# Optimization experiments

Measured on AMD Instinct MI355X. Metric: run time of the kernel, lower is better.

The kernel has to match this reference:

```python
import jax, jax.numpy as jnp
import numpy as np
import math

B, T, D, H = 4, 2048, 1024, 16
HD = D // H  # head_dim = 64

def setup_inputs() -> dict:
    key = jax.random.key(0)
    k1, k2, k3, k4, k5 = jax.random.split(key, 5)
    s = 1.0 / math.sqrt(D)
    return {
        "x": jax.random.normal(k1, (B, T, D), dtype=jnp.float32),
        "W_qkv": jax.random.normal(k2, (D, 3 * D), dtype=jnp.float32) * s,
        "b_qkv": jax.random.normal(k3, (3 * D,), dtype=jnp.float32) * 0.01,
        "W_fc": jax.random.normal(k4, (D, D), dtype=jnp.float32) * s,
        "b_fc": jax.random.normal(k5, (D,), dtype=jnp.float32) * 0.01,
    }

def reference(x, W_qkv, b_qkv, W_fc, b_fc):
    Bx, Tx, C = x.shape
    qkv = x @ W_qkv + b_qkv                                   # [B,T,3D]
    qkv = qkv.reshape(Bx, Tx, 3, H, HD)
    q, k, v = qkv[:, :, 0], qkv[:, :, 1], qkv[:, :, 2]        # [B,T,H,hd]
    scale = 1.0 / math.sqrt(HD)
    scores = jnp.einsum('bqhd,bkhd->bhqk', q, k) * scale      # [B,H,T,T]
    causal = jnp.tril(jnp.ones((Tx, Tx), dtype=bool))
    scores = jnp.where(causal, scores, -jnp.inf)
    weights = jax.nn.softmax(scores, axis=-1)
    out = jnp.einsum('bhqk,bkhd->bqhd', weights, v).reshape(Bx, Tx, C)
    return out @ W_fc + b_fc
```

## Files before the change

kernel.cpp:

```cpp
#include <hip/hip_runtime.h>
#include <hip/hip_bf16.h>

typedef __hip_bfloat16 bf16;
typedef short bf16x8 __attribute__((ext_vector_type(8)));
typedef float f32x4 __attribute__((ext_vector_type(4)));


static __device__ __forceinline__ void glds16(const bf16* g, bf16* l) {
  __builtin_amdgcn_global_load_lds(
      (const __attribute__((address_space(1))) void*)g,
      (__attribute__((address_space(3))) void*)l, 16, 0, 0);
}

static __device__ __forceinline__ unsigned short f2b(float f) {
  return __builtin_bit_cast(unsigned short, __float2bfloat16(f));
}
static __device__ __forceinline__ float b2f(unsigned int u16bits) {
  return __builtin_bit_cast(float, u16bits << 16);
}
static __device__ __forceinline__ float ex2(float x) {
  return __builtin_amdgcn_exp2f(x);
}

__global__ void k_convert(const float* __restrict__ in, unsigned short* __restrict__ out, int n4) {
  int i = blockIdx.x * 256 + threadIdx.x;
  if (i >= n4) return;
  float4 v = reinterpret_cast<const float4*>(in)[i];
  ushort4 o;
  o.x = f2b(v.x); o.y = f2b(v.y); o.z = f2b(v.z); o.w = f2b(v.w);
  reinterpret_cast<ushort4*>(out)[i] = o;
}

__global__ void k_transpose(const float* __restrict__ in, bf16* __restrict__ out, int R, int C) {
  __shared__ float t[32][33];
  int c0 = blockIdx.x * 32, r0 = blockIdx.y * 32;
  int tx = threadIdx.x, ty = threadIdx.y;
  #pragma unroll
  for (int j = 0; j < 32; j += 8)
    t[ty + j][tx] = in[(size_t)(r0 + ty + j) * C + c0 + tx];
  __syncthreads();
  #pragma unroll
  for (int j = 0; j < 32; j += 8)
    out[(size_t)(c0 + ty + j) * R + r0 + tx] = __float2bfloat16(t[tx][ty + j]);
}

template<int EPI>
__global__ __launch_bounds__(256, 2)
void k_gemm(const bf16* __restrict__ A, const bf16* __restrict__ Bt,
            const float* __restrict__ bias,
            bf16* __restrict__ Qh, bf16* __restrict__ Kh, bf16* __restrict__ Vt,
            float* __restrict__ Out)
{
  constexpr int K = 1024;
  __shared__ bf16 sA[128 * 64];
  __shared__ bf16 sB[128 * 64];
  const int tid = threadIdx.x;
  const int wv = tid >> 6, lane = tid & 63;
  const int wr = wv >> 1, wc = wv & 1;
  const int l4 = lane >> 4, l15 = lane & 15;

  const int nbx = gridDim.x;
  const int nwg = nbx * gridDim.y;
  const int flat = blockIdx.y * nbx + blockIdx.x;
  const int cpx = nwg >> 3;
  const int swz = (flat & 7) * cpx + (flat >> 3);
  const int bx = swz % nbx;
  const int by = swz / nbx;

  const int srow8 = lane >> 3;
  const int sgran = (lane & 7) ^ srow8;
  const bf16* gA0 = A  + (size_t)(by * 128 + wv * 8 + srow8) * K + sgran * 8;
  const bf16* gB0 = Bt + (size_t)(bx * 128 + wv * 8 + srow8) * K + sgran * 8;
  bf16* lA0 = sA + wv * 8 * 64;
  bf16* lB0 = sB + wv * 8 * 64;

  f32x4 acc[4][4];
  #pragma unroll
  for (int i = 0; i < 4; ++i)
    #pragma unroll
    for (int j = 0; j < 4; ++j) acc[i][j] = f32x4{0.f, 0.f, 0.f, 0.f};

  for (int kb = 0; kb < K; kb += 64) {
    #pragma unroll
    for (int c = 0; c < 4; ++c) {
      glds16(gA0 + kb + (size_t)(c * 32) * K, lA0 + c * 32 * 64);
      glds16(gB0 + kb + (size_t)(c * 32) * K, lB0 + c * 32 * 64);
    }
    __syncthreads();
    #pragma unroll
    for (int kk = 0; kk < 2; ++kk) {
      bf16x8 af[4], bfr[4];
      #pragma unroll
      for (int i = 0; i < 4; ++i) {
        const int R = wr * 64 + i * 16 + l15;
        af[i] = *reinterpret_cast<const bf16x8*>(
            sA + R * 64 + (((kk * 4 + l4) ^ (R & 7)) * 8));
      }
      #pragma unroll
      for (int j = 0; j < 4; ++j) {
        const int R = wc * 64 + j * 16 + l15;
        bfr[j] = *reinterpret_cast<const bf16x8*>(
            sB + R * 64 + (((kk * 4 + l4) ^ (R & 7)) * 8));
      }
      #pragma unroll
      for (int i = 0; i < 4; ++i)
        #pragma unroll
        for (int j = 0; j < 4; ++j)
          acc[i][j] = __builtin_amdgcn_mfma_f32_16x16x32_bf16(af[i], bfr[j], acc[i][j], 0, 0, 0);
    }
    __syncthreads();
  }

  if (EPI == 0) {
    #pragma unroll
    for (int j = 0; j < 4; ++j) {
      const int n = bx * 128 + wc * 64 + j * 16 + l15;
      const float bj = bias[n];
      const int s = n >> 10;
      const int hh = (n >> 6) & 15;
      const int d = n & 63;
      #pragma unroll
      for (int i = 0; i < 4; ++i) {
        #pragma unroll
        for (int r = 0; r < 4; ++r) {
          const int m = by * 128 + wr * 64 + i * 16 + l4 * 4 + r;
          const int bb = m >> 11, t = m & 2047;
          float of = acc[i][j][r] + bj;
          if (s == 0) of *= 0.18033688f;
          const bf16 o = __float2bfloat16(of);
          if (s == 0)      Qh[((size_t)((bb * 16 + hh) * 2048 + t)) * 64 + d] = o;
          else if (s == 1) Kh[((size_t)((bb * 16 + hh) * 2048 + t)) * 64 + d] = o;
          else             Vt[((size_t)((bb * 16 + hh) * 64 + d)) * 2048 + t] = o;
        }
      }
    }
  } else {
    #pragma unroll
    for (int j = 0; j < 4; ++j) {
      const int n = bx * 128 + wc * 64 + j * 16 + l15;
      const float bj = bias[n];
      #pragma unroll
      for (int i = 0; i < 4; ++i)
        #pragma unroll
        for (int r = 0; r < 4; ++r) {
          const int m = by * 128 + wr * 64 + i * 16 + l4 * 4 + r;
          Out[(size_t)m * 1024 + n] = acc[i][j][r] + bj;
        }
    }
  }
}

__global__ __launch_bounds__(256, 3)
void k_attn(const bf16* __restrict__ Qh, const bf16* __restrict__ Kh,
            const bf16* __restrict__ Vt, bf16* __restrict__ Ao)
{
  __shared__ unsigned int smem[4608];
  const int tid = threadIdx.x;
  const int wv = tid >> 6, lane = tid & 63;
  const int l4 = lane >> 4, l15 = lane & 15;

  const int bid = blockIdx.x;
  const int xcd = bid & 7;
  const int idx = bid >> 3;
  const int g   = idx & 31;
  const int grp = idx >> 5;
  const int bh  = grp * 8 + xcd;
  const int b = bh >> 4, h = bh & 15;

  const int role = (wv + bid) & 3;
  const int qi = (role < 2) ? g : (63 - g);
  const int parity = role & 1;
  const int qbase = qi * 32;

  const bf16* Qp = Qh + (size_t)bh * 2048 * 64;
  const bf16* Kp = Kh + (size_t)bh * 2048 * 64;
  const bf16* Vp = Vt + (size_t)bh * 64 * 2048;
  bf16* Pw = (bf16*)smem + wv * (32 * 40);

  bf16x8 qa[2][2];
  #pragma unroll
  for (int i = 0; i < 2; ++i)
    #pragma unroll
    for (int kh = 0; kh < 2; ++kh)
      qa[i][kh] = *reinterpret_cast<const bf16x8*>(
          Qp + (size_t)(qbase + i * 16 + l15) * 64 + kh * 32 + l4 * 8);

  f32x4 o[2][4];
  float mr[2], lr[2];
  #pragma unroll
  for (int i = 0; i < 2; ++i) {
    #pragma unroll
    for (int jd = 0; jd < 4; ++jd) o[i][jd] = f32x4{0.f, 0.f, 0.f, 0.f};
    mr[i] = -1e30f; lr[i] = 0.f;
  }

  const int ktmax = (qbase + 31) >> 5;

  const int kt0 = (parity <= ktmax) ? parity : ktmax;
  bf16x8 kbf[2][2];
  #pragma unroll
  for (int j = 0; j < 2; ++j)
    #pragma unroll
    for (int kh = 0; kh < 2; ++kh)
      kbf[j][kh] = *reinterpret_cast<const bf16x8*>(
          Kp + (size_t)(kt0 * 32 + j * 16 + l15) * 64 + kh * 32 + l4 * 8);

  for (int kt = parity; kt <= ktmax; kt += 2) {
    const bool full = (kt * 32 + 31) <= qbase;

    f32x4 s[2][2];
    #pragma unroll
    for (int i = 0; i < 2; ++i)
      #pragma unroll
      for (int j = 0; j < 2; ++j) s[i][j] = f32x4{0.f, 0.f, 0.f, 0.f};
    #pragma unroll
    for (int j = 0; j < 2; ++j)
      #pragma unroll
      for (int i = 0; i < 2; ++i) {
        s[i][j] = __builtin_amdgcn_mfma_f32_16x16x32_bf16(kbf[j][0], qa[i][0], s[i][j], 0, 0, 0);
        s[i][j] = __builtin_amdgcn_mfma_f32_16x16x32_bf16(kbf[j][1], qa[i][1], s[i][j], 0, 0, 0);
      }

    bf16x8 vbf[4];
    #pragma unroll
    for (int jd = 0; jd < 4; ++jd)
      vbf[jd] = *reinterpret_cast<const bf16x8*>(
          Vp + (size_t)(jd * 16 + l15) * 2048 + kt * 32 + l4 * 8);

    #pragma unroll
    for (int i = 0; i < 2; ++i) {
      const int q = qbase + i * 16 + l15;
      #pragma unroll
      for (int j = 0; j < 2; ++j)
        #pragma unroll
        for (int r = 0; r < 4; ++r) {
          float v = s[i][j][r];
          if (!full) {
            const int kk = kt * 32 + j * 16 + l4 * 4 + r;
            if (kk > q) v = -1e30f;
          }
          s[i][j][r] = v;
        }
    }

    #pragma unroll
    for (int i = 0; i < 2; ++i) {
      float mx = s[i][0][0];
      #pragma unroll
      for (int j = 0; j < 2; ++j)
        #pragma unroll
        for (int r = 0; r < 4; ++r)
          if (j + r > 0) mx = fmaxf(mx, s[i][j][r]);
      mx = fmaxf(mx, __shfl_xor(mx, 16));
      mx = fmaxf(mx, __shfl_xor(mx, 32));
      if (__any(mx > mr[i] + 8.f)) {
        const float mn = fmaxf(mr[i], mx);
        const float al = ex2(mr[i] - mn);
        mr[i] = mn;
        lr[i] *= al;
        float albc[4];
        #pragma unroll
        for (int r = 0; r < 4; ++r) albc[r] = __shfl(al, l4 * 4 + r);
        #pragma unroll
        for (int jd = 0; jd < 4; ++jd)
          #pragma unroll
          for (int r = 0; r < 4; ++r) o[i][jd][r] *= albc[r];
      }
      float ps = 0.f;
      #pragma unroll
      for (int j = 0; j < 2; ++j) {
        const float p0 = ex2(s[i][j][0] - mr[i]);
        const float p1 = ex2(s[i][j][1] - mr[i]);
        const float p2 = ex2(s[i][j][2] - mr[i]);
        const float p3 = ex2(s[i][j][3] - mr[i]);
        ps += (p0 + p1) + (p2 + p3);
        const unsigned int u0 = (unsigned int)f2b(p0) | ((unsigned int)f2b(p1) << 16);
        const unsigned int u1 = (unsigned int)f2b(p2) | ((unsigned int)f2b(p3) << 16);
        *reinterpret_cast<uint2*>(Pw + (i * 16 + l15) * 40 + j * 16 + l4 * 4) =
            make_uint2(u0, u1);
      }
      ps += __shfl_xor(ps, 16);
      ps += __shfl_xor(ps, 32);
      lr[i] += ps;
    }

    const int ktn = (kt + 2 <= ktmax) ? (kt + 2) : ktmax;
    #pragma unroll
    for (int j = 0; j < 2; ++j)
      #pragma unroll
      for (int kh = 0; kh < 2; ++kh)
        kbf[j][kh] = *reinterpret_cast<const bf16x8*>(
            Kp + (size_t)(ktn * 32 + j * 16 + l15) * 64 + kh * 32 + l4 * 8);

    bf16x8 pa[2];
    #pragma unroll
    for (int i = 0; i < 2; ++i)
      pa[i] = *reinterpret_cast<const bf16x8*>(Pw + (i * 16 + l15) * 40 + l4 * 8);
    #pragma unroll
    for (int jd = 0; jd < 4; ++jd)
      #pragma unroll
      for (int i = 0; i < 2; ++i)
        o[i][jd] = __builtin_amdgcn_mfma_f32_16x16x32_bf16(pa[i], vbf[jd], o[i][jd], 0, 0, 0);
  }

  float mrv[2][4], lrv[2][4];
  #pragma unroll
  for (int i = 0; i < 2; ++i)
    #pragma unroll
    for (int r = 0; r < 4; ++r) {
      mrv[i][r] = __shfl(mr[i], l4 * 4 + r);
      lrv[i][r] = __shfl(lr[i], l4 * 4 + r);
    }

  __syncthreads();
  unsigned int* reg0 = smem;
  unsigned int* reg1 = smem + 64 * 33;
  if (parity == 1) {
    unsigned int* p = ((role == 1) ? reg0 : reg1) + lane * 33;
    #pragma unroll
    for (int i = 0; i < 2; ++i)
      #pragma unroll
      for (int r = 0; r < 4; ++r) {
        p[i * 4 + r]     = __builtin_bit_cast(unsigned int, mrv[i][r]);
        p[8 + i * 4 + r] = __builtin_bit_cast(unsigned int, lrv[i][r]);
      }
    #pragma unroll
    for (int i = 0; i < 2; ++i)
      #pragma unroll
      for (int jd = 0; jd < 4; ++jd)
        #pragma unroll
        for (int rp = 0; rp < 2; ++rp) {
          unsigned int lo = f2b(o[i][jd][2 * rp]);
          unsigned int hi = f2b(o[i][jd][2 * rp + 1]);
          p[16 + (i * 4 + jd) * 2 + rp] = lo | (hi << 16);
        }
  }
  __syncthreads();
  if (parity == 0) {
    const unsigned int* p = ((role == 0) ? reg0 : reg1) + lane * 33;
    #pragma unroll
    for (int i = 0; i < 2; ++i)
      #pragma unroll
      for (int r = 0; r < 4; ++r) {
        const float m1 = __builtin_bit_cast(float, p[i * 4 + r]);
        const float l1 = __builtin_bit_cast(float, p[8 + i * 4 + r]);
        const float mm = fmaxf(mrv[i][r], m1);
        const float a0 = ex2(mrv[i][r] - mm);
        const float a1 = ex2(m1 - mm);
        const float inv = 1.f / (lrv[i][r] * a0 + l1 * a1);
        const int q = qbase + i * 16 + l4 * 4 + r;
        #pragma unroll
        for (int jd = 0; jd < 4; ++jd) {
          const unsigned int u = p[16 + (i * 4 + jd) * 2 + (r >> 1)];
          const float o1 = b2f((r & 1) ? (u >> 16) : (u & 0xffffu));
          const float val = (o[i][jd][r] * a0 + o1 * a1) * inv;
          Ao[(size_t)(b * 2048 + q) * 1024 + h * 64 + jd * 16 + l15] = __float2bfloat16(val);
        }
      }
  }
}

extern "C" void kernel_launch(void* const* d_in, const int* in_sizes, int n_in,
                              void* d_out, int out_size, void* d_ws, size_t ws_size,
                              hipStream_t stream)
{
  const float* x     = (const float*)d_in[0];
  const float* W_qkv = (const float*)d_in[1];
  const float* b_qkv = (const float*)d_in[2];
  const float* W_fc  = (const float*)d_in[3];
  const float* b_fc  = (const float*)d_in[4];
  float* out = (float*)d_out;

  char* ws = (char*)d_ws;
  bf16* x_bf = (bf16*)ws;  ws += (size_t)8192 * 1024 * 2;
  bf16* Wqt  = (bf16*)ws;  ws += (size_t)3072 * 1024 * 2;
  bf16* Wft  = (bf16*)ws;  ws += (size_t)1024 * 1024 * 2;
  bf16* Qh   = (bf16*)ws;  ws += (size_t)4 * 16 * 2048 * 64 * 2;
  bf16* Kh   = (bf16*)ws;  ws += (size_t)4 * 16 * 2048 * 64 * 2;
  bf16* Vt   = (bf16*)ws;  ws += (size_t)4 * 16 * 64 * 2048 * 2;
  bf16* Ao   = (bf16*)ws;  ws += (size_t)8192 * 1024 * 2;

  k_convert<<<8192, 256, 0, stream>>>(x, (unsigned short*)x_bf, 8192 * 1024 / 4);
  k_transpose<<<dim3(3072 / 32, 1024 / 32), dim3(32, 8), 0, stream>>>(W_qkv, Wqt, 1024, 3072);
  k_transpose<<<dim3(1024 / 32, 1024 / 32), dim3(32, 8), 0, stream>>>(W_fc, Wft, 1024, 1024);
  k_gemm<0><<<dim3(24, 64), 256, 0, stream>>>(x_bf, Wqt, b_qkv, Qh, Kh, Vt, nullptr);
  k_attn<<<2048, 256, 0, stream>>>(Qh, Kh, Vt, Ao);
  k_gemm<1><<<dim3(8, 64), 256, 0, stream>>>(Ao, Wft, b_fc, nullptr, nullptr, nullptr, out);
}
```

Measured before the change: 265.8 us.

## Replace QKV GEMM with 256x256-tile double-buffered pipelined kernel

The QKV projection moves to a new kernel with 256x256 output tiles, 8 waves per block and 128KB of dynamic LDS holding two K-stages. Global-to-LDS loads for the next stages are issued between MFMA phases, with explicit vmcnt waits, barriers and s_setprio, so memory traffic overlaps compute. The larger tile doubles reuse of each staged operand. The risks are one block per CU, higher register pressure from 32 accumulators per wave, and fragile hand-tuned wait counts. The output projection stays on the old kernel, now specialised as k_gemm_fc.

After: 268.7 us. Within noise of the previous version (+1.1%).

```diff
diff --git a/kernel.cpp b/kernel.cpp
--- a/kernel.cpp
+++ b/kernel.cpp
@@ -44,12 +44,135 @@
     out[(size_t)(c0 + ty + j) * R + r0 + tx] = __float2bfloat16(t[tx][ty + j]);
 }
 
-template<int EPI>
+__global__ __launch_bounds__(512, 1)
+void k_gemm2(const bf16* __restrict__ A, const bf16* __restrict__ Bt,
+             const float* __restrict__ bias,
+             bf16* __restrict__ Qh, bf16* __restrict__ Kh, bf16* __restrict__ Vt)
+{
+  constexpr int K = 1024, NT = 16;
+  extern __shared__ bf16 sm[];
+  #define BUFA(bb) (sm + (bb) * 2 * 16384)
+  #define BUFB(bb) (sm + (bb) * 2 * 16384 + 16384)
+
+  const int tid = threadIdx.x;
+  const int wv = tid >> 6, lane = tid & 63;
+  const int wr = wv >> 2, wc = wv & 3;
+  const int l4 = lane >> 4, l15 = lane & 15;
+
+  const int flat = blockIdx.x;
+  const int swz = (flat & 7) * 48 + (flat >> 3);
+  const int bx = swz % 12;
+  const int by = swz / 12;
+
+  const int srow = lane >> 3;
+  const int sgran = (lane & 7) ^ srow;
+  const bf16* gA = A  + (size_t)(by * 256 + wv * 8 + srow) * K + sgran * 8;
+  const bf16* gB = Bt + (size_t)(bx * 256 + wv * 8 + srow) * K + sgran * 8;
+
+  f32x4 acc[8][4];
+  #pragma unroll
+  for (int i = 0; i < 8; ++i)
+    #pragma unroll
+    for (int j = 0; j < 4; ++j) acc[i][j] = f32x4{0.f, 0.f, 0.f, 0.f};
+
+  #define STAGE_A(t, c, bb) glds16(gA + (size_t)((c) * 64) * K + (t) * 64, BUFA(bb) + ((c) * 64 + wv * 8) * 64)
+  #define STAGE_B(t, c, bb) glds16(gB + (size_t)((c) * 64) * K + (t) * 64, BUFB(bb) + ((c) * 64 + wv * 8) * 64)
+
+  #pragma unroll
+  for (int c = 0; c < 4; ++c) STAGE_A(0, c, 0);
+  #pragma unroll
+  for (int c = 0; c < 4; ++c) STAGE_B(0, c, 0);
+  #pragma unroll
+  for (int c = 0; c < 4; ++c) STAGE_B(1, c, 1);
+  STAGE_A(1, 0, 1);
+  STAGE_A(1, 2, 1);
+  asm volatile("s_waitcnt vmcnt(6)");
+  __builtin_amdgcn_sched_barrier(0);
+  __builtin_amdgcn_s_barrier();
+  __builtin_amdgcn_sched_barrier(0);
+
+  for (int h = 0; h < NT; ++h) {
+    const int b = h & 1;
+    bf16x8 bfr[4][2];
+    #pragma unroll
+    for (int p = 0; p < 4; ++p) {
+      if (p == 0) {
+        #pragma unroll
+        for (int j = 0; j < 4; ++j)
+          #pragma unroll
+          for (int kh = 0; kh < 2; ++kh) {
+            const int R = wc * 64 + j * 16 + l15;
+            bfr[j][kh] = *reinterpret_cast<const bf16x8*>(
+                BUFB(b) + R * 64 + (((kh * 4 + l4) ^ (R & 7)) * 8));
+          }
+      }
+      bf16x8 af[2][2];
+      #pragma unroll
+      for (int ii = 0; ii < 2; ++ii)
+        #pragma unroll
+        for (int kh = 0; kh < 2; ++kh) {
+          const int R = wr * 128 + p * 32 + ii * 16 + l15;
+          af[ii][kh] = *reinterpret_cast<const bf16x8*>(
+              BUFA(b) + R * 64 + (((kh * 4 + l4) ^ (R & 7)) * 8));
+        }
+      if (p == 0) { if (h + 1 < NT) { STAGE_A(h + 1, 1, b ^ 1); STAGE_A(h + 1, 3, b ^ 1); } }
+      if (p == 1) { if (h + 2 < NT) { STAGE_B(h + 2, 0, b);     STAGE_B(h + 2, 1, b);     } }
+      if (p == 2) { if (h + 2 < NT) { STAGE_B(h + 2, 2, b);     STAGE_B(h + 2, 3, b);     } }
+      if (p == 3) { if (h + 2 < NT) { STAGE_A(h + 2, 0, b);     STAGE_A(h + 2, 2, b);     } }
+      __builtin_amdgcn_s_barrier();
+      __builtin_amdgcn_sched_barrier(0);
+      asm volatile("s_waitcnt lgkmcnt(0)");
+      __builtin_amdgcn_sched_barrier(0);
+      __builtin_amdgcn_s_setprio(1);
+      #pragma unroll
+      for (int ii = 0; ii < 2; ++ii)
+        #pragma unroll
+        for (int j = 0; j < 4; ++j) {
+          acc[p * 2 + ii][j] = __builtin_amdgcn_mfma_f32_16x16x32_bf16(af[ii][0], bfr[j][0], acc[p * 2 + ii][j], 0, 0, 0);
+          acc[p * 2 + ii][j] = __builtin_amdgcn_mfma_f32_16x16x32_bf16(af[ii][1], bfr[j][1], acc[p * 2 + ii][j], 0, 0, 0);
+        }
+      __builtin_amdgcn_s_setprio(0);
+      if (p == 3) {
+        if (h < NT - 2) asm volatile("s_waitcnt vmcnt(6)");
+        else            asm volatile("s_waitcnt vmcnt(0)");
+        __builtin_amdgcn_sched_barrier(0);
+      }
+      __builtin_amdgcn_s_barrier();
+      __builtin_amdgcn_sched_barrier(0);
+    }
+  }
+  #undef STAGE_A
+  #undef STAGE_B
+  #undef BUFA
+  #undef BUFB
+
+  #pragma unroll
+  for (int j = 0; j < 4; ++j) {
+    const int n = bx * 256 + wc * 64 + j * 16 + l15;
+    const float bj = bias[n];
+    const int s = n >> 10;
+    const int hh = (n >> 6) & 15;
+    const int d = n & 63;
+    #pragma unroll
+    for (int i = 0; i < 8; ++i) {
+      #pragma unroll
+      for (int r = 0; r < 4; ++r) {
+        const int m = by * 256 + wr * 128 + i * 16 + l4 * 4 + r;
+        const int bb = m >> 11, t = m & 2047;
+        float of = acc[i][j][r] + bj;
+        if (s == 0) of *= 0.18033688f;
+        const bf16 o = __float2bfloat16(of);
+        if (s == 0)      Qh[((size_t)((bb * 16 + hh) * 2048 + t)) * 64 + d] = o;
+        else if (s == 1) Kh[((size_t)((bb * 16 + hh) * 2048 + t)) * 64 + d] = o;
+        else             Vt[((size_t)((bb * 16 + hh) * 64 + d)) * 2048 + t] = o;
+      }
+    }
+  }
+}
+
 __global__ __launch_bounds__(256, 2)
-void k_gemm(const bf16* __restrict__ A, const bf16* __restrict__ Bt,
-            const float* __restrict__ bias,
-            bf16* __restrict__ Qh, bf16* __restrict__ Kh, bf16* __restrict__ Vt,
-            float* __restrict__ Out)
+void k_gemm_fc(const bf16* __restrict__ A, const bf16* __restrict__ Bt,
+               const float* __restrict__ bias, float* __restrict__ Out)
 {
   constexpr int K = 1024;
   __shared__ bf16 sA[128 * 64];
@@ -93,14 +216,12 @@
       #pragma unroll
       for (int i = 0; i < 4; ++i) {
         const int R = wr * 64 + i * 16 + l15;
-        af[i] = *reinterpret_cast<const bf16x8*>(
-            sA + R * 64 + (((kk * 4 + l4) ^ (R & 7)) * 8));
+        af[i] = *reinterpret_cast<const bf16x8*>(sA + R * 64 + (((kk * 4 + l4) ^ (R & 7)) * 8));
       }
       #pragma unroll
       for (int j = 0; j < 4; ++j) {
         const int R = wc * 64 + j * 16 + l15;
-        bfr[j] = *reinterpret_cast<const bf16x8*>(
-            sB + R * 64 + (((kk * 4 + l4) ^ (R & 7)) * 8));
+        bfr[j] = *reinterpret_cast<const bf16x8*>(sB + R * 64 + (((kk * 4 + l4) ^ (R & 7)) * 8));
       }
       #pragma unroll
       for (int i = 0; i < 4; ++i)
@@ -111,42 +232,17 @@
     __syncthreads();
   }
 
-  if (EPI == 0) {
-    #pragma unroll
-    for (int j = 0; j < 4; ++j) {
-      const int n = bx * 128 + wc * 64 + j * 16 + l15;
-      const float bj = bias[n];
-      const int s = n >> 10;
-      const int hh = (n >> 6) & 15;
-      const int d = n & 63;
-      #pragma unroll
-      for (int i = 0; i < 4; ++i) {
-        #pragma unroll
-        for (int r = 0; r < 4; ++r) {
-          const int m = by * 128 + wr * 64 + i * 16 + l4 * 4 + r;
-          const int bb = m >> 11, t = m & 2047;
-          float of = acc[i][j][r] + bj;
-          if (s == 0) of *= 0.18033688f;
-          const bf16 o = __float2bfloat16(of);
-          if (s == 0)      Qh[((size_t)((bb * 16 + hh) * 2048 + t)) * 64 + d] = o;
-          else if (s == 1) Kh[((size_t)((bb * 16 + hh) * 2048 + t)) * 64 + d] = o;
-          else             Vt[((size_t)((bb * 16 + hh) * 64 + d)) * 2048 + t] = o;
-        }
-      }
-    }
-  } else {
-    #pragma unroll
-    for (int j = 0; j < 4; ++j) {
-      const int n = bx * 128 + wc * 64 + j * 16 + l15;
-      const float bj = bias[n];
-      #pragma unroll
-      for (int i = 0; i < 4; ++i)
-        #pragma unroll
-        for (int r = 0; r < 4; ++r) {
-          const int m = by * 128 + wr * 64 + i * 16 + l4 * 4 + r;
-          Out[(size_t)m * 1024 + n] = acc[i][j][r] + bj;
-        }
-    }
+  #pragma unroll
+  for (int j = 0; j < 4; ++j) {
+    const int n = bx * 128 + wc * 64 + j * 16 + l15;
+    const float bj = bias[n];
+    #pragma unroll
+    for (int i = 0; i < 4; ++i)
+      #pragma unroll
+      for (int r = 0; r < 4; ++r) {
+        const int m = by * 128 + wr * 64 + i * 16 + l4 * 4 + r;
+        Out[(size_t)m * 1024 + n] = acc[i][j][r] + bj;
+      }
   }
 }
 
@@ -380,10 +476,13 @@
   bf16* Vt   = (bf16*)ws;  ws += (size_t)4 * 16 * 64 * 2048 * 2;
   bf16* Ao   = (bf16*)ws;  ws += (size_t)8192 * 1024 * 2;
 
+  (void)hipFuncSetAttribute((const void*)k_gemm2,
+                            hipFuncAttributeMaxDynamicSharedMemorySize, 131072);
+
   k_convert<<<8192, 256, 0, stream>>>(x, (unsigned short*)x_bf, 8192 * 1024 / 4);
   k_transpose<<<dim3(3072 / 32, 1024 / 32), dim3(32, 8), 0, stream>>>(W_qkv, Wqt, 1024, 3072);
   k_transpose<<<dim3(1024 / 32, 1024 / 32), dim3(32, 8), 0, stream>>>(W_fc, Wft, 1024, 1024);
-  k_gemm<0><<<dim3(24, 64), 256, 0, stream>>>(x_bf, Wqt, b_qkv, Qh, Kh, Vt, nullptr);
+  k_gemm2<<<384, 512, 131072, stream>>>(x_bf, Wqt, b_qkv, Qh, Kh, Vt);
   k_attn<<<2048, 256, 0, stream>>>(Qh, Kh, Vt, Ao);
-  k_gemm<1><<<dim3(8, 64), 256, 0, stream>>>(Ao, Wft, b_fc, nullptr, nullptr, nullptr, out);
-}
+  k_gemm_fc<<<dim3(8, 64), 256, 0, stream>>>(Ao, Wft, b_fc, out);
+}
```
